# Kernel optimization log

Measured on AMD Instinct MI355X. Metric: run time of the kernel, lower is better.

The kernel has to match this reference:

```python
import jax, jax.numpy as jnp
import numpy as np

NUM_GRAPHS = 64
NUM_LAYERS = 3
HEADS = 4
HID = 64
DMODEL = HEADS * HID  # 256
NUM_EDGE_TYPES = 8
NUM_CLASSES = 2
N_NODES = 30000
N_EDGES = 240000


def setup_inputs() -> dict:
    key = jax.random.key(0)
    ks = jax.random.split(key, 16)
    s = 0.05
    x = jax.random.normal(ks[0], (N_NODES, DMODEL), jnp.float32)
    edge_index = jax.random.randint(ks[1], (2, N_EDGES), 0, N_NODES)
    batch = jnp.sort(jax.random.randint(ks[2], (N_NODES,), 0, NUM_GRAPHS))
    edge_type_ids = jax.random.randint(ks[3], (N_EDGES,), 0, NUM_EDGE_TYPES)
    # stacked per-layer conv params (all layers are DMODEL -> HEADS*HID = DMODEL)
    Wq = jax.random.normal(ks[4], (NUM_LAYERS, DMODEL, DMODEL), jnp.float32) * s
    bq = jax.random.normal(ks[5], (NUM_LAYERS, DMODEL), jnp.float32) * s
    Wk = jax.random.normal(ks[6], (NUM_LAYERS, DMODEL, DMODEL), jnp.float32) * s
    bk = jax.random.normal(ks[7], (NUM_LAYERS, DMODEL), jnp.float32) * s
    Wv = jax.random.normal(ks[8], (NUM_LAYERS, DMODEL, DMODEL), jnp.float32) * s
    bv = jax.random.normal(ks[9], (NUM_LAYERS, DMODEL), jnp.float32) * s
    Eemb = jax.random.normal(ks[10], (NUM_LAYERS, NUM_EDGE_TYPES, DMODEL), jnp.float32) * s
    # 1-layer GRU (PyTorch layout: [3*hid, in], gate order r, z, n)
    W_ih = jax.random.normal(ks[11], (3 * HID, DMODEL), jnp.float32) * s
    b_ih = jax.random.normal(ks[12], (3 * HID,), jnp.float32) * s
    W_hh = jax.random.normal(ks[13], (3 * HID, HID), jnp.float32) * s
    b_hh = jax.random.normal(ks[14], (3 * HID,), jnp.float32) * s
    W_fc = jax.random.normal(ks[15], (NUM_CLASSES, HID), jnp.float32) * s
    b_fc = jnp.zeros((NUM_CLASSES,), jnp.float32)
    return dict(x=x, edge_index=edge_index, batch=batch, edge_type_ids=edge_type_ids,
                Wq=Wq, bq=bq, Wk=Wk, bk=bk, Wv=Wv, bv=bv, Eemb=Eemb,
                W_ih=W_ih, b_ih=b_ih, W_hh=W_hh, b_hh=b_hh, W_fc=W_fc, b_fc=b_fc)


def reference(x, edge_index, batch, edge_type_ids, Wq, bq, Wk, bk, Wv, bv, Eemb,
              W_ih, b_ih, W_hh, b_hh, W_fc, b_fc):
    N = x.shape[0]
    src, dst = edge_index[0], edge_index[1]  # messages flow src -> dst
    scale = 1.0 / jnp.sqrt(jnp.float32(HID))
    for l in range(NUM_LAYERS):
        q = (x @ Wq[l] + bq[l]).reshape(N, HEADS, HID)
        k_all = x @ Wk[l] + bk[l]  # [N, DMODEL]
        v_all = x @ Wv[l] + bv[l]
        ete = Eemb[l][edge_type_ids]  # edge-type conditioning, [E, DMODEL]
        k = (k_all[src] + ete).reshape(-1, HEADS, HID)
        v = (v_all[src] + ete).reshape(-1, HEADS, HID)
        scores = jnp.einsum('ehd,ehd->eh', q[dst], k) * scale  # [E, H]
        # per-destination-node segment softmax (stable)
        m = jax.ops.segment_max(scores, dst, num_segments=N)
        ex = jnp.exp(scores - m[dst])
        den = jax.ops.segment_sum(ex, dst, num_segments=N)
        alpha = ex / (den[dst] + 1e-16)
        agg = jax.ops.segment_sum(alpha[..., None] * v, dst, num_segments=N)
        x = jax.nn.elu(agg.reshape(N, DMODEL))
    # global mean pool over graphs
    cnt = jax.ops.segment_sum(jnp.ones((N,), x.dtype), batch, num_segments=NUM_GRAPHS)
    g = jax.ops.segment_sum(x, batch, num_segments=NUM_GRAPHS) / jnp.maximum(cnt, 1.0)[:, None]
    # single GRU step from h0 = 0 (seq_len == 1)
    h0 = jnp.zeros((NUM_GRAPHS, HID), x.dtype)
    gi = g @ W_ih.T + b_ih
    gh = h0 @ W_hh.T + b_hh
    ir, iz, inn = jnp.split(gi, 3, axis=-1)
    hr, hz, hn = jnp.split(gh, 3, axis=-1)
    r = jax.nn.sigmoid(ir + hr)
    z = jax.nn.sigmoid(iz + hz)
    n = jnp.tanh(inn + r * hn)
    h = (1.0 - z) * n + z * h0
    return h @ W_fc.T + b_fc  # [NUM_GRAPHS, NUM_CLASSES]
```

## Files before the change

### kernel.cpp

```cpp
#include <hip/hip_runtime.h>
#include <math.h>

#define N_NODES 30000
#define N_EDGES 240000
#define DMODEL 256
#define NETYPES 8
#define NGRAPHS 64
#define NLAYERS 3

typedef __attribute__((ext_vector_type(8))) short short8;
typedef __attribute__((ext_vector_type(8))) unsigned short ushort8;
typedef __attribute__((ext_vector_type(4))) float f32x4;

__device__ __forceinline__ unsigned short f2bf(float f) {
  union { float f; unsigned u; } v; v.f = f;
  unsigned r = v.u + 0x7FFF + ((v.u >> 16) & 1);
  return (unsigned short)(r >> 16);
}
__device__ __forceinline__ float bf2f(unsigned short h) {
  union { unsigned u; float f; } v; v.u = ((unsigned)h) << 16;
  return v.f;
}

__device__ __forceinline__ void async_g2l(const unsigned short* g, unsigned short* l) {
  __builtin_amdgcn_global_load_lds(
      (const __attribute__((address_space(1))) void*)g,
      (__attribute__((address_space(3))) void*)l, 16, 0, 0);
}

__device__ __forceinline__ float dpp_red_add(float x) {
  int v = __float_as_int(x);
  int t;
  t = __builtin_amdgcn_update_dpp(0, v, 0xB1, 0xF, 0xF, true);
  v = __float_as_int(__int_as_float(v) + __int_as_float(t));
  t = __builtin_amdgcn_update_dpp(0, v, 0x4E, 0xF, 0xF, true);
  v = __float_as_int(__int_as_float(v) + __int_as_float(t));
  t = __builtin_amdgcn_update_dpp(0, v, 0x141, 0xF, 0xF, true);
  v = __float_as_int(__int_as_float(v) + __int_as_float(t));
  t = __builtin_amdgcn_update_dpp(0, v, 0x140, 0xF, 0xF, true);
  v = __float_as_int(__int_as_float(v) + __int_as_float(t));
  return __int_as_float(v);
}

__global__ void k_count_deg(const int* __restrict__ dst, int* __restrict__ deg) {
  int e = blockIdx.x * blockDim.x + threadIdx.x;
  if (e < N_EDGES) atomicAdd(&deg[dst[e]], 1);
}

__global__ __launch_bounds__(1024) void k_scan(const int* __restrict__ deg,
                                               int* __restrict__ rowstart,
                                               int* __restrict__ cursor) {
  const int C = 30;
  int tid = threadIdx.x;
  int base = tid * C;
  int vals[C];
  int sum = 0;
#pragma unroll
  for (int j = 0; j < C; ++j) {
    int idx = base + j;
    int v = (idx < N_NODES) ? deg[idx] : 0;
    vals[j] = sum;
    sum += v;
  }
  int lane = tid & 63, wv = tid >> 6;
  int s = sum;
#pragma unroll
  for (int off = 1; off < 64; off <<= 1) {
    int t2 = __shfl_up(s, off);
    if (lane >= off) s += t2;
  }
  __shared__ int wsum[16];
  if (lane == 63) wsum[wv] = s;
  __syncthreads();
  if (tid == 0) {
    int a = 0;
#pragma unroll
    for (int i = 0; i < 16; ++i) { int t2 = wsum[i]; wsum[i] = a; a += t2; }
    rowstart[N_NODES] = a;
  }
  __syncthreads();
  int texcl = wsum[wv] + (s - sum);
#pragma unroll
  for (int j = 0; j < C; ++j) {
    int idx = base + j;
    if (idx < N_NODES) {
      int p = texcl + vals[j];
      rowstart[idx] = p;
      cursor[idx]   = p;
    }
  }
}

__global__ void k_scatter(const int* __restrict__ src, const int* __restrict__ dst,
                          const int* __restrict__ etype, int* __restrict__ cursor,
                          int* __restrict__ packed) {
  int e = blockIdx.x * blockDim.x + threadIdx.x;
  if (e < N_EDGES) {
    int p = atomicAdd(&cursor[dst[e]], 1);
    packed[p] = src[e] * NETYPES + etype[e];
  }
}

__global__ __launch_bounds__(256) void k_cvt_w(
    const float* __restrict__ Wq, const float* __restrict__ Wk, const float* __restrict__ Wv,
    unsigned short* __restrict__ wthi) {
  __shared__ float tile[32][33];
  int k0 = blockIdx.x * 32;
  int n0g = blockIdx.y * 32;
  int l = blockIdx.z;
  int which = n0g >> 8;
  int col0 = n0g & 255;
  const float* W = (which == 0) ? Wq : ((which == 1) ? Wk : Wv);
  int c = threadIdx.x & 31, r = threadIdx.x >> 5;
#pragma unroll
  for (int rr = 0; rr < 4; ++rr) {
    int kk = r + rr * 8;
    tile[kk][c] = W[(size_t)l * 65536 + (size_t)(k0 + kk) * 256 + col0 + c];
  }
  __syncthreads();
  int kk = threadIdx.x & 31, nn0 = threadIdx.x >> 5;
#pragma unroll
  for (int rr = 0; rr < 4; ++rr) {
    int nn = nn0 + rr * 8;
    wthi[((size_t)l * 768 + n0g + nn) * 256 + k0 + kk] = f2bf(tile[kk][nn]);
  }
}

__global__ void k_cvt_b(const float* __restrict__ bq, const float* __restrict__ bk,
                        const float* __restrict__ bv, float* __restrict__ bcat) {
  int idx = blockIdx.x * 256 + threadIdx.x;
  if (idx >= NLAYERS * 768) return;
  int n = idx % 768, l = idx / 768;
  int which = n >> 8, col = n & 255;
  const float* b = (which == 0) ? bq : ((which == 1) ? bk : bv);
  bcat[idx] = b[l * 256 + col];
}

__global__ void k_cvt_x(const float* __restrict__ x, unsigned short* __restrict__ xhi,
                        unsigned short* __restrict__ xlo) {
  int i = blockIdx.x * 256 + threadIdx.x;
  if (i < N_NODES * 256) {
    float v = x[i];
    unsigned short h = f2bf(v);
    xhi[i] = h;
    xlo[i] = f2bf(v - bf2f(h));
  }
}

__global__ __launch_bounds__(256, 5) void k_gemm_mfma(
    const unsigned short* __restrict__ Ahi, const unsigned short* __restrict__ Alo,
    const unsigned short* __restrict__ Bhi,
    const float* __restrict__ bcat, float* __restrict__ qbuf,
    unsigned short* __restrict__ kv) {
  __shared__ unsigned short smem[2 * 8192];

  int tid = threadIdx.x;
  int lane = tid & 63, wave = tid >> 6;
  int bx = blockIdx.x;
  int xcd = bx & 7, slot = bx >> 3;
  int rt = xcd + (slot / 6) * 8;
  if (rt >= 469) return;
  int row0 = rt * 64;
  int n0 = (slot % 6) * 128;
  int wm = (wave >> 1) * 32, wn = (wave & 1) * 64;
  int quad = lane >> 4, l16 = lane & 15;
  int lrow = lane >> 2;
  int chSw = (lane & 3) ^ ((lane >> 3) & 3);
  int rdSw = (quad ^ ((l16 >> 1) & 3)) * 8;

  f32x4 acc[2][4];
#pragma unroll
  for (int i = 0; i < 2; ++i)
#pragma unroll
    for (int j = 0; j < 4; ++j) acc[i][j] = (f32x4)(0.f);

  auto STAGE = [&](int k0, int b) {
    unsigned short* s = smem + b * 8192;
    int garA = row0 + wave * 16 + lrow; if (garA >= N_NODES) garA = N_NODES - 1;
    size_t acol = (size_t)garA * 256 + k0 + chSw * 8;
    async_g2l(Ahi + acol, s + wave * 512);
    async_g2l(Alo + acol, s + 2048 + wave * 512);
#pragma unroll
    for (int r = 0; r < 2; ++r) {
      int brow = r * 64 + wave * 16 + lrow;
      size_t boff = (size_t)(n0 + brow) * 256 + k0 + chSw * 8;
      async_g2l(Bhi + boff, s + 4096 + r * 2048 + wave * 512);
    }
  };

  STAGE(0, 0);
#pragma unroll
  for (int k = 0; k < 8; ++k) {
    int cur = k & 1;
    if (k < 7) {
      STAGE((k + 1) * 32, cur ^ 1);
      asm volatile("s_waitcnt vmcnt(4)" ::: "memory");
    } else {
      asm volatile("s_waitcnt vmcnt(0)" ::: "memory");
    }
    __builtin_amdgcn_s_barrier();

    const unsigned short* sAhi = smem + cur * 8192;
    const unsigned short* sAlo = sAhi + 2048;
    const unsigned short* sB   = sAhi + 4096;
    short8 ah[2], al[2], bh[4];
#pragma unroll
    for (int i = 0; i < 2; ++i) {
      int off = (wm + i * 16 + l16) * 32 + rdSw;
      ah[i] = *(const short8*)(sAhi + off);
      al[i] = *(const short8*)(sAlo + off);
    }
#pragma unroll
    for (int j = 0; j < 4; ++j) {
      int off = (wn + j * 16 + l16) * 32 + rdSw;
      bh[j] = *(const short8*)(sB + off);
    }
#pragma unroll
    for (int i = 0; i < 2; ++i)
#pragma unroll
      for (int j = 0; j < 4; ++j) {
        acc[i][j] = __builtin_amdgcn_mfma_f32_16x16x32_bf16(ah[i], bh[j], acc[i][j], 0, 0, 0);
        acc[i][j] = __builtin_amdgcn_mfma_f32_16x16x32_bf16(al[i], bh[j], acc[i][j], 0, 0, 0);
      }
    __builtin_amdgcn_s_barrier();
  }

  float bj[4];
#pragma unroll
  for (int j = 0; j < 4; ++j) bj[j] = bcat[n0 + wn + j * 16 + l16];
  bool isq = (n0 < 256);
  int cb = n0 - 256;
  int isV = cb >> 8;
  int cc0 = (cb & 255) + wn + l16;
#pragma unroll
  for (int i = 0; i < 2; ++i) {
    int rowb = row0 + wm + i * 16 + quad * 4;
#pragma unroll
    for (int r = 0; r < 4; ++r) {
      int grow = rowb + r;
      if (grow < N_NODES) {
        if (isq) {
          float* cp = qbuf + (size_t)grow * 256 + n0 + wn + l16;
#pragma unroll
          for (int j = 0; j < 4; ++j) cp[j * 16] = acc[i][j][r] + bj[j];
        } else {
          unsigned short* rowp = kv + (size_t)grow * 512 + isV * 4;
#pragma unroll
          for (int j = 0; j < 4; ++j) {
            int c = cc0 + j * 16;
            rowp[((c >> 2) << 3) + (c & 3)] = f2bf(acc[i][j][r] + bj[j]);
          }
        }
      }
    }
  }
}

#define GATHER(PK) (((const ushort8*)(kv + (size_t)((PK) >> 3) * 512))[lane])

#define PROC(PK, C)                                                      \
  { float4 e4 = ((const float4*)(ete_s + ((PK) & 7) * 256))[lane];       \
    float p_ = (bf2f(C[0]) + e4.x) * q4.x + (bf2f(C[1]) + e4.y) * q4.y + \
               (bf2f(C[2]) + e4.z) * q4.z + (bf2f(C[3]) + e4.w) * q4.w;  \
    p_ = dpp_red_add(p_);                                                \
    float e1_ = __expf(p_ * 0.125f);                                     \
    lsum += e1_;                                                         \
    ax = fmaf(e1_, bf2f(C[4]) + e4.x, ax);                               \
    ay = fmaf(e1_, bf2f(C[5]) + e4.y, ay);                               \
    az = fmaf(e1_, bf2f(C[6]) + e4.z, az);                               \
    aw = fmaf(e1_, bf2f(C[7]) + e4.w, aw); }

__global__ __launch_bounds__(256) void k_attn(
    const float* __restrict__ qbuf, const unsigned short* __restrict__ kv,
    const int* __restrict__ rowstart, const int* __restrict__ packed,
    const float* __restrict__ Eemb_l,
    unsigned short* __restrict__ xhi, unsigned short* __restrict__ xlo) {
  __shared__ float ete_s[NETYPES * 256];
  __shared__ int pk_s[512];
  int t = threadIdx.x;
#pragma unroll
  for (int i = 0; i < NETYPES; ++i) ete_s[i * 256 + t] = Eemb_l[i * 256 + t];
  int nb = blockIdx.x * 4;
  int brs = rowstart[nb], bre = rowstart[nb + 4];
  int cnt = bre - brs;
  if (cnt <= 512) {
    for (int j = t; j < cnt; j += 256) pk_s[j] = packed[brs + j];
  }
  __syncthreads();
  int lane = t & 63;
  int n = nb + (t >> 6);
  float4 q4 = ((const float4*)(qbuf + (size_t)n * 256))[lane];
  int rs = rowstart[n], re = rowstart[n + 1];
  float lsum = 0.f, ax = 0.f, ay = 0.f, az = 0.f, aw = 0.f;

  if (cnt <= 512) {
    int i0 = rs - brs, ie = re - brs;
    int m = ie - i0;
    int npair = m >> 1;
    int pkA0 = 0, pkB0 = 0, pkA1 = 0, pkB1 = 0;
    ushort8 cA0 = (ushort8)(unsigned short)0, cB0 = cA0, cA1 = cA0, cB1 = cA0;
    if (npair >= 1) {
      pkA0 = pk_s[i0]; pkB0 = pk_s[i0 + 1];
      cA0 = GATHER(pkA0); cB0 = GATHER(pkB0);
    }
    for (int p = 0; p < npair; ++p) {
      int nx = i0 + 2 * p + 2;
      if ((p & 1) == 0) {
        if (p + 1 < npair) {
          pkA1 = pk_s[nx]; pkB1 = pk_s[nx + 1];
          cA1 = GATHER(pkA1); cB1 = GATHER(pkB1);
        }
        PROC(pkA0, cA0) PROC(pkB0, cB0)
      } else {
        if (p + 1 < npair) {
          pkA0 = pk_s[nx]; pkB0 = pk_s[nx + 1];
          cA0 = GATHER(pkA0); cB0 = GATHER(pkB0);
        }
        PROC(pkA1, cA1) PROC(pkB1, cB1)
      }
    }
    if (m & 1) {
      int pk = pk_s[ie - 1];
      ushort8 c = GATHER(pk);
      PROC(pk, c)
    }
  } else {
    for (int i = rs; i < re; ++i) {
      int pk = packed[i];
      ushort8 c = GATHER(pk);
      PROC(pk, c)
    }
  }

  float inv = 1.f / (lsum + 1e-16f);
  float4 o;
  o.x = ax * inv; o.y = ay * inv;
  o.z = az * inv; o.w = aw * inv;
  o.x = o.x > 0.f ? o.x : expm1f(o.x);
  o.y = o.y > 0.f ? o.y : expm1f(o.y);
  o.z = o.z > 0.f ? o.z : expm1f(o.z);
  o.w = o.w > 0.f ? o.w : expm1f(o.w);
  unsigned short h0 = f2bf(o.x), h1 = f2bf(o.y), h2 = f2bf(o.z), h3 = f2bf(o.w);
  ushort4 hv, lv;
  hv.x = h0; hv.y = h1; hv.z = h2; hv.w = h3;
  lv.x = f2bf(o.x - bf2f(h0)); lv.y = f2bf(o.y - bf2f(h1));
  lv.z = f2bf(o.z - bf2f(h2)); lv.w = f2bf(o.w - bf2f(h3));
  size_t base_o = (size_t)n * 256 + lane * 4;
  *(ushort4*)(xhi + base_o) = hv;
  *(ushort4*)(xlo + base_o) = lv;
}

__global__ __launch_bounds__(256) void k_pool_partial(
    const unsigned short* __restrict__ xhi, const unsigned short* __restrict__ xlo,
    const int* __restrict__ batch, float* __restrict__ gacc) {
  int t = threadIdx.x;
  int base = blockIdx.x * 128;
  int end = base + 128; if (end > N_NODES) end = N_NODES;
  __shared__ int bsh[128];
  if (t < 128 && base + t < N_NODES) bsh[t] = batch[base + t];
  __syncthreads();
  float acc = 0.f;
  int cur = bsh[0];
  for (int n = base; n < end; ++n) {
    int g = bsh[n - base];
    if (g != cur) {
      atomicAdd(&gacc[cur * 256 + t], acc);
      acc = 0.f; cur = g;
    }
    size_t idx = (size_t)n * 256 + t;
    acc += bf2f(xhi[idx]) + bf2f(xlo[idx]);
  }
  atomicAdd(&gacc[cur * 256 + t], acc);
}

__device__ inline int lower_bound_dev(const int* a, int n, int val) {
  int lo = 0, hi = n;
  while (lo < hi) {
    int mid = (lo + hi) >> 1;
    if (a[mid] < val) lo = mid + 1; else hi = mid;
  }
  return lo;
}

__global__ __launch_bounds__(256) void k_gru_fc(
    const float* __restrict__ gacc, const int* __restrict__ batch,
    const float* __restrict__ W_ih, const float* __restrict__ b_ih,
    const float* __restrict__ b_hh, const float* __restrict__ W_fc,
    const float* __restrict__ b_fc, float* __restrict__ out) {
  __shared__ float gv[256];
  __shared__ float gates[192];
  __shared__ float h[64];
  int gr = blockIdx.x, t = threadIdx.x;
  int s0 = lower_bound_dev(batch, N_NODES, gr);
  int e0 = lower_bound_dev(batch, N_NODES, gr + 1);
  float c = (e0 > s0) ? (float)(e0 - s0) : 1.f;
  gv[t] = gacc[gr * 256 + t] / c;
  __syncthreads();
  if (t < 192) {
    const float* wr = W_ih + t * 256;
    float s = b_ih[t];
    for (int k = 0; k < 256; ++k) s = fmaf(gv[k], wr[k], s);
    gates[t] = s;
  }
  __syncthreads();
  if (t < 64) {
    float r  = 1.f / (1.f + expf(-(gates[t] + b_hh[t])));
    float z  = 1.f / (1.f + expf(-(gates[64 + t] + b_hh[64 + t])));
    float nn = tanhf(gates[128 + t] + r * b_hh[128 + t]);
    h[t] = (1.f - z) * nn;
  }
  __syncthreads();
  if (t < 2) {
    const float* wr = W_fc + t * 64;
    float s = b_fc[t];
    for (int k = 0; k < 64; ++k) s = fmaf(h[k], wr[k], s);
    out[gr * 2 + t] = s;
  }
}

extern "C" void kernel_launch(void* const* d_in, const int* in_sizes, int n_in,
                              void* d_out, int out_size, void* d_ws, size_t ws_size,
                              hipStream_t stream) {
  const float* x     = (const float*)d_in[0];
  const int* edge_index = (const int*)d_in[1];
  const int* batch   = (const int*)d_in[2];
  const int* etype   = (const int*)d_in[3];
  const float* Wq    = (const float*)d_in[4];
  const float* bq    = (const float*)d_in[5];
  const float* Wk    = (const float*)d_in[6];
  const float* bk    = (const float*)d_in[7];
  const float* Wv    = (const float*)d_in[8];
  const float* bv    = (const float*)d_in[9];
  const float* Eemb  = (const float*)d_in[10];
  const float* W_ih  = (const float*)d_in[11];
  const float* b_ih  = (const float*)d_in[12];
  const float* b_hh  = (const float*)d_in[14];
  const float* W_fc  = (const float*)d_in[15];
  const float* b_fc  = (const float*)d_in[16];
  float* out = (float*)d_out;

  const int* src = edge_index;
  const int* dst = edge_index + N_EDGES;

  float* qbuf  = (float*)d_ws;
  float* gacc  = qbuf + (size_t)N_NODES * 256;
  float* bcat  = gacc + NGRAPHS * 256;
  unsigned short* kv   = (unsigned short*)(bcat + NLAYERS * 768);
  unsigned short* xhi  = kv + (size_t)N_NODES * 512;
  unsigned short* xlo  = xhi + (size_t)N_NODES * 256;
  unsigned short* wthi = xlo + (size_t)N_NODES * 256;
  int* deg      = (int*)(wthi + (size_t)NLAYERS * 768 * 256);
  int* rowstart = deg + N_NODES;
  int* cursor   = rowstart + N_NODES + 1;
  int* packed   = cursor + N_NODES;

  hipMemsetAsync(deg, 0, N_NODES * sizeof(int), stream);
  hipMemsetAsync(gacc, 0, NGRAPHS * 256 * sizeof(float), stream);
  k_count_deg<<<(N_EDGES + 255) / 256, 256, 0, stream>>>(dst, deg);
  k_scan<<<1, 1024, 0, stream>>>(deg, rowstart, cursor);
  k_scatter<<<(N_EDGES + 255) / 256, 256, 0, stream>>>(src, dst, etype, cursor, packed);

  k_cvt_w<<<dim3(8, 24, 3), 256, 0, stream>>>(Wq, Wk, Wv, wthi);
  k_cvt_b<<<(NLAYERS * 768 + 255) / 256, 256, 0, stream>>>(bq, bk, bv, bcat);
  k_cvt_x<<<(N_NODES * 256 + 255) / 256, 256, 0, stream>>>(x, xhi, xlo);

  for (int l = 0; l < NLAYERS; ++l) {
    k_gemm_mfma<<<59 * 8 * 6, 256, 0, stream>>>(
        xhi, xlo, wthi + (size_t)l * 768 * 256,
        bcat + l * 768, qbuf, kv);
    k_attn<<<N_NODES / 4, 256, 0, stream>>>(qbuf, kv, rowstart, packed,
                                            Eemb + (size_t)l * NETYPES * 256, xhi, xlo);
  }
  k_pool_partial<<<(N_NODES + 127) / 128, 256, 0, stream>>>(xhi, xlo, batch, gacc);
  k_gru_fc<<<NGRAPHS, 256, 0, stream>>>(gacc, batch, W_ih, b_ih, b_hh, W_fc, b_fc, out);
}
```

Before: 460.3 us.

## Fuse prep kernels and sort attention nodes by degree for load balance

Merges the degree count, x/W/bias conversion and gacc zeroing into one multi-role prep kernel, which cuts launch count and replaces a memset. The scan kernel now also builds a degree-descending permutation with a shared histogram counting sort, and the attention kernel processes nodes in that order so each block's four waves have similar edge counts. The attention loop drops the LDS staging of packed indices and the software-pipelined gather in favour of two independent accumulator chains read directly from global memory. That trade may expose more gather latency and scatters output writes, while the single-block sort adds serial work.

```diff
diff --git a/kernel.cpp b/kernel.cpp
--- a/kernel.cpp
+++ b/kernel.cpp
@@ -42,14 +42,82 @@
   return __int_as_float(v);
 }
 
-__global__ void k_count_deg(const int* __restrict__ dst, int* __restrict__ deg) {
-  int e = blockIdx.x * blockDim.x + threadIdx.x;
-  if (e < N_EDGES) atomicAdd(&deg[dst[e]], 1);
-}
-
-__global__ __launch_bounds__(1024) void k_scan(const int* __restrict__ deg,
-                                               int* __restrict__ rowstart,
-                                               int* __restrict__ cursor) {
+#define PREP_CNT 938
+#define PREP_CVTX 3750
+#define PREP_CVTW 576
+#define PREP_CVTB 9
+#define PREP_GACC 64
+#define B_CVTX (PREP_CNT)
+#define B_CVTW (B_CVTX + PREP_CVTX)
+#define B_CVTB (B_CVTW + PREP_CVTW)
+#define B_GACC (B_CVTB + PREP_CVTB)
+#define PREP_BLOCKS (B_GACC + PREP_GACC)
+
+__global__ __launch_bounds__(256) void k_prep(
+    const int* __restrict__ dst, int* __restrict__ deg,
+    const float* __restrict__ x, unsigned short* __restrict__ xhi,
+    unsigned short* __restrict__ xlo,
+    const float* __restrict__ Wq, const float* __restrict__ Wk,
+    const float* __restrict__ Wv, unsigned short* __restrict__ wthi,
+    const float* __restrict__ bq, const float* __restrict__ bk,
+    const float* __restrict__ bv, float* __restrict__ bcat,
+    float* __restrict__ gacc) {
+  __shared__ float tile[32][33];
+  int bid = blockIdx.x, t = threadIdx.x;
+  if (bid < PREP_CNT) {
+    int e = bid * 256 + t;
+    if (e < N_EDGES) atomicAdd(&deg[dst[e]], 1);
+  } else if (bid < B_CVTW) {
+    size_t i0 = ((size_t)(bid - B_CVTX) * 256 + t) * 8;
+#pragma unroll
+    for (int h = 0; h < 2; ++h) {
+      float4 v4 = *(const float4*)(x + i0 + h * 4);
+      ushort4 hv, lv;
+      hv.x = f2bf(v4.x); lv.x = f2bf(v4.x - bf2f(hv.x));
+      hv.y = f2bf(v4.y); lv.y = f2bf(v4.y - bf2f(hv.y));
+      hv.z = f2bf(v4.z); lv.z = f2bf(v4.z - bf2f(hv.z));
+      hv.w = f2bf(v4.w); lv.w = f2bf(v4.w - bf2f(hv.w));
+      *(ushort4*)(xhi + i0 + h * 4) = hv;
+      *(ushort4*)(xlo + i0 + h * 4) = lv;
+    }
+  } else if (bid < B_CVTB) {
+    int rel = bid - B_CVTW;
+    int k0 = (rel & 7) * 32;
+    int n0g = ((rel >> 3) % 24) * 32;
+    int l = rel / 192;
+    int which = n0g >> 8;
+    int col0 = n0g & 255;
+    const float* W = (which == 0) ? Wq : ((which == 1) ? Wk : Wv);
+    int c = t & 31, r = t >> 5;
+#pragma unroll
+    for (int rr = 0; rr < 4; ++rr) {
+      int kk = r + rr * 8;
+      tile[kk][c] = W[(size_t)l * 65536 + (size_t)(k0 + kk) * 256 + col0 + c];
+    }
+    __syncthreads();
+    int kk = t & 31, nn0 = t >> 5;
+#pragma unroll
+    for (int rr = 0; rr < 4; ++rr) {
+      int nn = nn0 + rr * 8;
+      wthi[((size_t)l * 768 + n0g + nn) * 256 + k0 + kk] = f2bf(tile[kk][nn]);
+    }
+  } else if (bid < B_GACC) {
+    int idx = (bid - B_CVTB) * 256 + t;
+    if (idx < NLAYERS * 768) {
+      int n = idx % 768, l = idx / 768;
+      int which = n >> 8, col = n & 255;
+      const float* b = (which == 0) ? bq : ((which == 1) ? bk : bv);
+      bcat[idx] = b[l * 256 + col];
+    }
+  } else {
+    int idx = (bid - B_GACC) * 256 + t;
+    gacc[idx] = 0.f;
+  }
+}
+
+__global__ __launch_bounds__(1024) void k_scan_sort(
+    const int* __restrict__ deg, int* __restrict__ rowstart,
+    int* __restrict__ cursor, int* __restrict__ perm) {
   const int C = 30;
   int tid = threadIdx.x;
   int base = tid * C;
@@ -87,6 +155,32 @@
       int p = texcl + vals[j];
       rowstart[idx] = p;
       cursor[idx]   = p;
+    }
+  }
+  __shared__ int hist[256], bstart[256], bcur[256];
+  if (tid < 256) hist[tid] = 0;
+  __syncthreads();
+  for (int j = 0; j < C; ++j) {
+    int idx = base + j;
+    if (idx < N_NODES) {
+      int d = deg[idx]; if (d > 255) d = 255;
+      atomicAdd(&hist[d], 1);
+    }
+  }
+  __syncthreads();
+  if (tid == 0) {
+    int a = 0;
+    for (int b = 255; b >= 0; --b) { bstart[b] = a; a += hist[b]; }
+  }
+  __syncthreads();
+  if (tid < 256) bcur[tid] = bstart[tid];
+  __syncthreads();
+  for (int j = 0; j < C; ++j) {
+    int idx = base + j;
+    if (idx < N_NODES) {
+      int d = deg[idx]; if (d > 255) d = 255;
+      int pos = atomicAdd(&bcur[d], 1);
+      perm[pos] = idx;
     }
   }
 }
@@ -98,52 +192,6 @@
   if (e < N_EDGES) {
     int p = atomicAdd(&cursor[dst[e]], 1);
     packed[p] = src[e] * NETYPES + etype[e];
-  }
-}
-
-__global__ __launch_bounds__(256) void k_cvt_w(
-    const float* __restrict__ Wq, const float* __restrict__ Wk, const float* __restrict__ Wv,
-    unsigned short* __restrict__ wthi) {
-  __shared__ float tile[32][33];
-  int k0 = blockIdx.x * 32;
-  int n0g = blockIdx.y * 32;
-  int l = blockIdx.z;
-  int which = n0g >> 8;
-  int col0 = n0g & 255;
-  const float* W = (which == 0) ? Wq : ((which == 1) ? Wk : Wv);
-  int c = threadIdx.x & 31, r = threadIdx.x >> 5;
-#pragma unroll
-  for (int rr = 0; rr < 4; ++rr) {
-    int kk = r + rr * 8;
-    tile[kk][c] = W[(size_t)l * 65536 + (size_t)(k0 + kk) * 256 + col0 + c];
-  }
-  __syncthreads();
-  int kk = threadIdx.x & 31, nn0 = threadIdx.x >> 5;
-#pragma unroll
-  for (int rr = 0; rr < 4; ++rr) {
-    int nn = nn0 + rr * 8;
-    wthi[((size_t)l * 768 + n0g + nn) * 256 + k0 + kk] = f2bf(tile[kk][nn]);
-  }
-}
-
-__global__ void k_cvt_b(const float* __restrict__ bq, const float* __restrict__ bk,
-                        const float* __restrict__ bv, float* __restrict__ bcat) {
-  int idx = blockIdx.x * 256 + threadIdx.x;
-  if (idx >= NLAYERS * 768) return;
-  int n = idx % 768, l = idx / 768;
-  int which = n >> 8, col = n & 255;
-  const float* b = (which == 0) ? bq : ((which == 1) ? bk : bv);
-  bcat[idx] = b[l * 256 + col];
-}
-
-__global__ void k_cvt_x(const float* __restrict__ x, unsigned short* __restrict__ xhi,
-                        unsigned short* __restrict__ xlo) {
-  int i = blockIdx.x * 256 + threadIdx.x;
-  if (i < N_NODES * 256) {
-    float v = x[i];
-    unsigned short h = f2bf(v);
-    xhi[i] = h;
-    xlo[i] = f2bf(v - bf2f(h));
   }
 }
 
@@ -256,86 +304,66 @@
   }
 }
 
-#define GATHER(PK) (((const ushort8*)(kv + (size_t)((PK) >> 3) * 512))[lane])
-
-#define PROC(PK, C)                                                      \
-  { float4 e4 = ((const float4*)(ete_s + ((PK) & 7) * 256))[lane];       \
-    float p_ = (bf2f(C[0]) + e4.x) * q4.x + (bf2f(C[1]) + e4.y) * q4.y + \
-               (bf2f(C[2]) + e4.z) * q4.z + (bf2f(C[3]) + e4.w) * q4.w;  \
-    p_ = dpp_red_add(p_);                                                \
-    float e1_ = __expf(p_ * 0.125f);                                     \
-    lsum += e1_;                                                         \
-    ax = fmaf(e1_, bf2f(C[4]) + e4.x, ax);                               \
-    ay = fmaf(e1_, bf2f(C[5]) + e4.y, ay);                               \
-    az = fmaf(e1_, bf2f(C[6]) + e4.z, az);                               \
-    aw = fmaf(e1_, bf2f(C[7]) + e4.w, aw); }
-
 __global__ __launch_bounds__(256) void k_attn(
     const float* __restrict__ qbuf, const unsigned short* __restrict__ kv,
     const int* __restrict__ rowstart, const int* __restrict__ packed,
-    const float* __restrict__ Eemb_l,
+    const int* __restrict__ perm, const float* __restrict__ Eemb_l,
     unsigned short* __restrict__ xhi, unsigned short* __restrict__ xlo) {
   __shared__ float ete_s[NETYPES * 256];
-  __shared__ int pk_s[512];
   int t = threadIdx.x;
 #pragma unroll
   for (int i = 0; i < NETYPES; ++i) ete_s[i * 256 + t] = Eemb_l[i * 256 + t];
-  int nb = blockIdx.x * 4;
-  int brs = rowstart[nb], bre = rowstart[nb + 4];
-  int cnt = bre - brs;
-  if (cnt <= 512) {
-    for (int j = t; j < cnt; j += 256) pk_s[j] = packed[brs + j];
-  }
   __syncthreads();
   int lane = t & 63;
-  int n = nb + (t >> 6);
+  int n = perm[blockIdx.x * 4 + (t >> 6)];
   float4 q4 = ((const float4*)(qbuf + (size_t)n * 256))[lane];
   int rs = rowstart[n], re = rowstart[n + 1];
-  float lsum = 0.f, ax = 0.f, ay = 0.f, az = 0.f, aw = 0.f;
-
-  if (cnt <= 512) {
-    int i0 = rs - brs, ie = re - brs;
-    int m = ie - i0;
-    int npair = m >> 1;
-    int pkA0 = 0, pkB0 = 0, pkA1 = 0, pkB1 = 0;
-    ushort8 cA0 = (ushort8)(unsigned short)0, cB0 = cA0, cA1 = cA0, cB1 = cA0;
-    if (npair >= 1) {
-      pkA0 = pk_s[i0]; pkB0 = pk_s[i0 + 1];
-      cA0 = GATHER(pkA0); cB0 = GATHER(pkB0);
-    }
-    for (int p = 0; p < npair; ++p) {
-      int nx = i0 + 2 * p + 2;
-      if ((p & 1) == 0) {
-        if (p + 1 < npair) {
-          pkA1 = pk_s[nx]; pkB1 = pk_s[nx + 1];
-          cA1 = GATHER(pkA1); cB1 = GATHER(pkB1);
-        }
-        PROC(pkA0, cA0) PROC(pkB0, cB0)
-      } else {
-        if (p + 1 < npair) {
-          pkA0 = pk_s[nx]; pkB0 = pk_s[nx + 1];
-          cA0 = GATHER(pkA0); cB0 = GATHER(pkB0);
-        }
-        PROC(pkA1, cA1) PROC(pkB1, cB1)
-      }
-    }
-    if (m & 1) {
-      int pk = pk_s[ie - 1];
-      ushort8 c = GATHER(pk);
-      PROC(pk, c)
-    }
-  } else {
-    for (int i = rs; i < re; ++i) {
-      int pk = packed[i];
-      ushort8 c = GATHER(pk);
-      PROC(pk, c)
-    }
-  }
-
-  float inv = 1.f / (lsum + 1e-16f);
+  float l1 = 0.f, ax1 = 0.f, ay1 = 0.f, az1 = 0.f, aw1 = 0.f;
+  float l2 = 0.f, ax2 = 0.f, ay2 = 0.f, az2 = 0.f, aw2 = 0.f;
+  int i = rs;
+  for (; i + 2 <= re; i += 2) {
+    int pkA = packed[i], pkB = packed[i + 1];
+    ushort8 cA = ((const ushort8*)(kv + (size_t)(pkA >> 3) * 512))[lane];
+    ushort8 cB = ((const ushort8*)(kv + (size_t)(pkB >> 3) * 512))[lane];
+    float4 eA = ((const float4*)(ete_s + (pkA & 7) * 256))[lane];
+    float4 eB = ((const float4*)(ete_s + (pkB & 7) * 256))[lane];
+    float pA = (bf2f(cA[0]) + eA.x) * q4.x + (bf2f(cA[1]) + eA.y) * q4.y +
+               (bf2f(cA[2]) + eA.z) * q4.z + (bf2f(cA[3]) + eA.w) * q4.w;
+    float pB = (bf2f(cB[0]) + eB.x) * q4.x + (bf2f(cB[1]) + eB.y) * q4.y +
+               (bf2f(cB[2]) + eB.z) * q4.z + (bf2f(cB[3]) + eB.w) * q4.w;
+    pA = dpp_red_add(pA);
+    pB = dpp_red_add(pB);
+    float e1 = __expf(pA * 0.125f);
+    float e2 = __expf(pB * 0.125f);
+    l1 += e1; l2 += e2;
+    ax1 = fmaf(e1, bf2f(cA[4]) + eA.x, ax1);
+    ay1 = fmaf(e1, bf2f(cA[5]) + eA.y, ay1);
+    az1 = fmaf(e1, bf2f(cA[6]) + eA.z, az1);
+    aw1 = fmaf(e1, bf2f(cA[7]) + eA.w, aw1);
+    ax2 = fmaf(e2, bf2f(cB[4]) + eB.x, ax2);
+    ay2 = fmaf(e2, bf2f(cB[5]) + eB.y, ay2);
+    az2 = fmaf(e2, bf2f(cB[6]) + eB.z, az2);
+    aw2 = fmaf(e2, bf2f(cB[7]) + eB.w, aw2);
+  }
+  if (i < re) {
+    int pk = packed[i];
+    ushort8 c = ((const ushort8*)(kv + (size_t)(pk >> 3) * 512))[lane];
+    float4 e4 = ((const float4*)(ete_s + (pk & 7) * 256))[lane];
+    float p = (bf2f(c[0]) + e4.x) * q4.x + (bf2f(c[1]) + e4.y) * q4.y +
+              (bf2f(c[2]) + e4.z) * q4.z + (bf2f(c[3]) + e4.w) * q4.w;
+    p = dpp_red_add(p);
+    float e1 = __expf(p * 0.125f);
+    l1 += e1;
+    ax1 = fmaf(e1, bf2f(c[4]) + e4.x, ax1);
+    ay1 = fmaf(e1, bf2f(c[5]) + e4.y, ay1);
+    az1 = fmaf(e1, bf2f(c[6]) + e4.z, az1);
+    aw1 = fmaf(e1, bf2f(c[7]) + e4.w, aw1);
+  }
+  float l = l1 + l2;
+  float inv = 1.f / (l + 1e-16f);
   float4 o;
-  o.x = ax * inv; o.y = ay * inv;
-  o.z = az * inv; o.w = aw * inv;
+  o.x = (ax1 + ax2) * inv; o.y = (ay1 + ay2) * inv;
+  o.z = (az1 + az2) * inv; o.w = (aw1 + aw2) * inv;
   o.x = o.x > 0.f ? o.x : expm1f(o.x);
   o.y = o.y > 0.f ? o.y : expm1f(o.y);
   o.z = o.z > 0.f ? o.z : expm1f(o.z);
@@ -453,22 +481,19 @@
   int* rowstart = deg + N_NODES;
   int* cursor   = rowstart + N_NODES + 1;
   int* packed   = cursor + N_NODES;
+  int* perm     = packed + N_EDGES;
 
   hipMemsetAsync(deg, 0, N_NODES * sizeof(int), stream);
-  hipMemsetAsync(gacc, 0, NGRAPHS * 256 * sizeof(float), stream);
-  k_count_deg<<<(N_EDGES + 255) / 256, 256, 0, stream>>>(dst, deg);
-  k_scan<<<1, 1024, 0, stream>>>(deg, rowstart, cursor);
+  k_prep<<<PREP_BLOCKS, 256, 0, stream>>>(dst, deg, x, xhi, xlo,
+                                          Wq, Wk, Wv, wthi, bq, bk, bv, bcat, gacc);
+  k_scan_sort<<<1, 1024, 0, stream>>>(deg, rowstart, cursor, perm);
   k_scatter<<<(N_EDGES + 255) / 256, 256, 0, stream>>>(src, dst, etype, cursor, packed);
-
-  k_cvt_w<<<dim3(8, 24, 3), 256, 0, stream>>>(Wq, Wk, Wv, wthi);
-  k_cvt_b<<<(NLAYERS * 768 + 255) / 256, 256, 0, stream>>>(bq, bk, bv, bcat);
-  k_cvt_x<<<(N_NODES * 256 + 255) / 256, 256, 0, stream>>>(x, xhi, xlo);
 
   for (int l = 0; l < NLAYERS; ++l) {
     k_gemm_mfma<<<59 * 8 * 6, 256, 0, stream>>>(
         xhi, xlo, wthi + (size_t)l * 768 * 256,
         bcat + l * 768, qbuf, kv);
-    k_attn<<<N_NODES / 4, 256, 0, stream>>>(qbuf, kv, rowstart, packed,
+    k_attn<<<N_NODES / 4, 256, 0, stream>>>(qbuf, kv, rowstart, packed, perm,
                                             Eemb + (size_t)l * NETYPES * 256, xhi, xlo);
   }
   k_pool_partial<<<(N_NODES + 127) / 128, 256, 0, stream>>>(xhi, xlo, batch, gacc);
```

New measurement: 487.8 us. 1.06x slower.
